# Performance work log

Hardware: AMD Instinct MI355X
Metric: run time of the kernel (lower is better)

The kernel has to match this reference:

```python
import jax, jax.numpy as jnp
import numpy as np

N_NODES = 100000
N_EDGES = 3200000
IN_F = 128
OUT_F = 64
HEADS = 8
ALPHA = 0.2  # LeakyReLU negative slope


def setup_inputs() -> dict:
    key = jax.random.key(0)
    k1, k2, k3, k4 = jax.random.split(key, 4)
    x = jax.random.normal(k1, (N_NODES, IN_F), dtype=jnp.float32)
    edges = jax.random.randint(k2, (2, N_EDGES), 0, N_NODES, dtype=jnp.int64)
    # glorot-uniform-ish scaled params, stacked over heads
    lim_W = np.sqrt(6.0 / (IN_F + OUT_F))
    lim_a = np.sqrt(6.0 / (2 * OUT_F + 1))
    W = jax.random.uniform(k3, (HEADS, IN_F, OUT_F), minval=-lim_W, maxval=lim_W, dtype=jnp.float32)
    a = jax.random.uniform(k4, (HEADS, 2 * OUT_F, 1), minval=-lim_a, maxval=lim_a, dtype=jnp.float32)
    return {"x": x, "edges": edges, "W": W, "a": a}


def reference(x, edges, W, a):
    # x: [N, in_f]; edges: [2, E]; W: [H, in_f, out_f]; a: [H, 2*out_f, 1]
    N = x.shape[0]
    src, tgt = edges[0], edges[1]
    outs = []
    for h in range(W.shape[0]):  # small fixed head count; keeps peak memory per-head
        Wh = x @ W[h]                                  # [N, F]
        # Whij @ a == Wh[src] @ a[:F] + Wh[tgt] @ a[F:], computed at node level
        a_src = Wh @ a[h, :OUT_F, 0]                   # [N]
        a_tgt = Wh @ a[h, OUT_F:, 0]                   # [N]
        e = -jax.nn.leaky_relu(a_src[src] + a_tgt[tgt], negative_slope=ALPHA)  # [E]
        e_exp = jnp.exp(e - jnp.max(e))                # global max, as in the torch code
        denom = jax.ops.segment_sum(e_exp, src, num_segments=N) + 1e-10  # [N]
        att = e_exp / denom[src]                       # [E] edge softmax over source groups
        msg = att[:, None] * Wh[tgt]                   # [E, F]
        outs.append(jax.ops.segment_sum(msg, src, num_segments=N))  # [N, F]
    return jnp.concatenate(outs, axis=1)               # concat reduction -> [N, H*F]
```

## Files before the change

### kernel.cpp

```cpp
#include <hip/hip_runtime.h>
#include <hip/hip_bf16.h>

#define N_NODES 100000
#define N_EDGES 3200000
#define IN_F 128
#define OUT_F 64
#define HEADS 8
#define ALPHA 0.2f

#define BSHIFT 7
#define NBUCK 782
#define CHUNK 2048
#define NPBLK 1563
#define XADOT_BLKS 1024

typedef __bf16 bf16x8 __attribute__((ext_vector_type(8)));
typedef float f32x4 __attribute__((ext_vector_type(4)));
typedef __attribute__((ext_vector_type(8))) unsigned short ushort8;

static __device__ __forceinline__ unsigned short f2b(float f) {
    __hip_bfloat16 h = __float2bfloat16(f);
    return __builtin_bit_cast(unsigned short, h);
}

static __device__ __forceinline__ void gll16(const void* g, void* l) {
    __builtin_amdgcn_global_load_lds(
        (const __attribute__((address_space(1))) void*)g,
        (__attribute__((address_space(3))) void*)l, 16, 0, 0);
}

__global__ __launch_bounds__(256) void k_prep(const float* __restrict__ W,
                                              const float* __restrict__ a,
                                              unsigned short* __restrict__ Wt,
                                              float* __restrict__ uvT,
                                              int* __restrict__ bhist) {
    int b = blockIdx.x, t = threadIdx.x;
    if (b < 256) {
        int idx = b * 256 + t;
        int k = idx & 127;
        int c = idx >> 7;
        int h = c >> 6;
        int f = c & 63;
        Wt[idx] = f2b(W[h * IN_F * OUT_F + k * OUT_F + f]);
    } else if (b == 256) {
#pragma unroll
        for (int j = 0; j < 4; ++j) {
            int t2 = t + j * 256;
            int h = t2 >> 7, k = t2 & 127;
            const float* Wrow = W + h * IN_F * OUT_F + k * OUT_F;
            const float* ah = a + h * 2 * OUT_F;
            float su = 0.f, sv = 0.f;
            for (int f = 0; f < OUT_F; ++f) {
                float wv = Wrow[f];
                su += wv * ah[f];
                sv += wv * ah[OUT_F + f];
            }
            uvT[k * 16 + h] = su;
            uvT[k * 16 + 8 + h] = sv;
        }
    } else {
        for (int i = t; i < NBUCK; i += 256) bhist[i] = 0;
    }
}

__global__ __launch_bounds__(256) void k_xadot(const float* __restrict__ x,
                                               const float* __restrict__ uvT,
                                               const int* __restrict__ src,
                                               unsigned short* __restrict__ xb,
                                               float* __restrict__ asrc,
                                               float* __restrict__ atgt,
                                               int* __restrict__ bhist) {
    const int b = blockIdx.x, t = threadIdx.x;
    if (b >= XADOT_BLKS) {
        __shared__ int h[NBUCK];
        for (int i = t; i < NBUCK; i += 256) h[i] = 0;
        __syncthreads();
        int cb = b - XADOT_BLKS;
        int i0 = cb * CHUNK;
        int iend = i0 + CHUNK;
        if (iend > N_EDGES) iend = N_EDGES;
        for (int i = i0 + t; i < iend; i += 256)
            atomicAdd(&h[src[i] >> BSHIFT], 1);
        __syncthreads();
        for (int i = t; i < NBUCK; i += 256)
            if (h[i]) atomicAdd(&bhist[i], h[i]);
        return;
    }
    const int lane = t & 63, wid = t >> 6;
    const int o = lane & 15, q = lane >> 4;
    float up[32];
#pragma unroll
    for (int j = 0; j < 32; ++j) up[j] = uvT[(q * 32 + j) * 16 + o];

    for (int n = b * 4 + wid; n < N_NODES; n += XADOT_BLKS * 4) {
        const float* xr = x + (size_t)n * 128;
        float2 xv2 = *reinterpret_cast<const float2*>(xr + 2 * lane);
        ushort2 pv = make_ushort2(f2b(xv2.x), f2b(xv2.y));
        *reinterpret_cast<ushort2*>(xb + (size_t)n * 128 + 2 * lane) = pv;
        float r = 0.f;
        const float4* xq = reinterpret_cast<const float4*>(xr + q * 32);
#pragma unroll
        for (int j = 0; j < 8; ++j) {
            float4 xv = xq[j];
            r = fmaf(xv.x, up[4 * j], r);
            r = fmaf(xv.y, up[4 * j + 1], r);
            r = fmaf(xv.z, up[4 * j + 2], r);
            r = fmaf(xv.w, up[4 * j + 3], r);
        }
        r += __shfl_xor(r, 16);
        r += __shfl_xor(r, 32);
        if (lane < 8) asrc[n * 8 + o] = r;
        else if (lane < 16) atgt[n * 8 + (o - 8)] = r;
    }
}

__global__ __launch_bounds__(1024) void k_bscan(const int* __restrict__ bhist,
                                                int* __restrict__ bstart,
                                                int* __restrict__ bcursor,
                                                int* __restrict__ rowptr) {
    __shared__ int s[1024];
    int t = threadIdx.x;
    int v = (t < NBUCK) ? bhist[t] : 0;
    s[t] = v;
    __syncthreads();
    for (int d = 1; d < 1024; d <<= 1) {
        int add = (t >= d) ? s[t - d] : 0;
        __syncthreads();
        s[t] += add;
        __syncthreads();
    }
    if (t < NBUCK) {
        int st = s[t] - v;
        bstart[t] = st;
        bcursor[t] = st;
    }
    if (t == 0) {
        bstart[NBUCK] = N_EDGES;
        rowptr[N_NODES] = N_EDGES;
    }
}

__global__ __launch_bounds__(256) void k_bscatter(const int* __restrict__ src,
                                                  const int* __restrict__ tgt,
                                                  int* __restrict__ bcursor,
                                                  unsigned int* __restrict__ pairs) {
    __shared__ int h[NBUCK];
    __shared__ int rsv[NBUCK];
    for (int i = threadIdx.x; i < NBUCK; i += 256) h[i] = 0;
    __syncthreads();
    int i0 = blockIdx.x * CHUNK;
    int iend = i0 + CHUNK;
    if (iend > N_EDGES) iend = N_EDGES;
    for (int i = i0 + threadIdx.x; i < iend; i += 256)
        atomicAdd(&h[src[i] >> BSHIFT], 1);
    __syncthreads();
    for (int i = threadIdx.x; i < NBUCK; i += 256) {
        int c = h[i];
        rsv[i] = c ? atomicAdd(&bcursor[i], c) : 0;
        h[i] = 0;
    }
    __syncthreads();
    for (int i = i0 + threadIdx.x; i < iend; i += 256) {
        int s = src[i];
        int b = s >> BSHIFT;
        int p = rsv[b] + atomicAdd(&h[b], 1);
        pairs[p] = ((unsigned)(s & 127) << 17) | (unsigned)tgt[i];
    }
}

__global__ __launch_bounds__(512) void k_bsort(const unsigned int* __restrict__ pairs,
                                               const int* __restrict__ bstart,
                                               int* __restrict__ rowptr,
                                               int* __restrict__ stgt) {
    __shared__ int h[128];
    __shared__ int s[128];
    int b = blockIdx.x;
    int p0 = bstart[b], p1 = bstart[b + 1];
    int n0 = b << BSHIFT;
    int t = threadIdx.x;
    if (t < 128) h[t] = 0;
    __syncthreads();
    for (int i = p0 + t; i < p1; i += 512)
        atomicAdd(&h[pairs[i] >> 17], 1);
    __syncthreads();
    int v = (t < 128) ? h[t] : 0;
    if (t < 128) s[t] = v;
    __syncthreads();
    for (int d = 1; d < 128; d <<= 1) {
        int add = (t >= d && t < 128) ? s[t - d] : 0;
        __syncthreads();
        if (t < 128) s[t] += add;
        __syncthreads();
    }
    if (t < 128) {
        int pos = p0 + s[t] - v;
        int node = n0 + t;
        if (node < N_NODES) rowptr[node] = pos;
        h[t] = pos;
    }
    __syncthreads();
    for (int i = p0 + t; i < p1; i += 512) {
        unsigned int pr = pairs[i];
        int pos = atomicAdd(&h[pr >> 17], 1);
        stgt[pos] = (int)(pr & 0x1FFFF);
    }
}

__global__ __launch_bounds__(256) void k_agg10(const int* __restrict__ rowptr,
                                               const int* __restrict__ stgt,
                                               const float* __restrict__ asrc,
                                               const float* __restrict__ atgt,
                                               const unsigned short* __restrict__ xb,
                                               unsigned short* __restrict__ aggout) {
    __shared__ char lds[4 * 5120];
    const int tid = threadIdx.x;
    const int wid = tid >> 6, lane = tid & 63;
    const int node = blockIdx.x * 4 + wid;
    if (node >= N_NODES) return;
    const int seg = lane & 15;
    const int hp = lane >> 4;
    const int base = rowptr[node], end = rowptr[node + 1];
    const float2 asr = *reinterpret_cast<const float2*>(asrc + (size_t)node * 8 + hp * 2);
    char* buf = lds + wid * 5120;

    float2 accA[4] = {}, accB[4] = {};
    float den0 = 0.f, den1 = 0.f;

    const int deg = end - base;
    const int nch = (deg + 15) >> 4;

    auto eidx = [&](int c) {
        int i = base + c * 16 + seg;
        if (i >= end) i = end - 1;
        return i;
    };
    auto stage = [&](int t16) {
        int te_a = __shfl(t16, (lane & 31) >> 1);
        gll16(atgt + (size_t)te_a * 8 + (lane & 1) * 4, buf);
#pragma unroll
        for (int p = 0; p < 4; ++p) {
            int te = __shfl(t16, p * 4 + hp);
            gll16(xb + (size_t)te * 128 + seg * 8, buf + 1024 + p * 1024);
        }
    };

#define EDGE_STEP(E) { \
        uint4 xu = *reinterpret_cast<const uint4*>(Xb + (E) * 256 + seg * 16); \
        float2 w2 = *reinterpret_cast<const float2*>(buf + (E) * 32 + hp * 8); \
        _Pragma("unroll") \
        for (int i = 0; i < 4; ++i) { \
            unsigned int u = (&xu.x)[i]; \
            float2 xv; \
            xv.x = __builtin_bit_cast(float, u << 16); \
            xv.y = __builtin_bit_cast(float, u & 0xFFFF0000u); \
            asm("v_pk_fma_f32 %0, %1, %2, %0 op_sel:[0,0,0] op_sel_hi:[1,0,1]" \
                : "+v"(accA[i]) : "v"(xv), "v"(w2)); \
            asm("v_pk_fma_f32 %0, %1, %2, %0 op_sel:[0,1,0] op_sel_hi:[1,1,1]" \
                : "+v"(accB[i]) : "v"(xv), "v"(w2)); \
        } }

    if (nch > 0) {
        int t16 = stgt[eidx(0)];
        for (int c = 0; c < nch; ++c) {
            asm volatile("s_waitcnt lgkmcnt(0)" ::: "memory");
            __builtin_amdgcn_sched_barrier(0);
            stage(t16);
            if (c + 1 < nch) t16 = stgt[eidx(c + 1)];
            asm volatile("s_waitcnt vmcnt(0)" ::: "memory");
            __builtin_amdgcn_sched_barrier(0);
            int c0 = base + c * 16;
            int cnt = end - c0;
            if (cnt > 16) cnt = 16;
            {
                float2 at2 = *reinterpret_cast<const float2*>(buf + seg * 32 + hp * 8);
                float z0 = asr.x + at2.x, z1 = asr.y + at2.y;
                float e0 = (z0 > 0.f) ? -z0 : -(ALPHA * z0);
                float e1 = (z1 > 0.f) ? -z1 : -(ALPHA * z1);
                bool ok = seg < cnt;
                float w0 = ok ? __expf(e0) : 0.f;
                float w1 = ok ? __expf(e1) : 0.f;
                den0 += w0;
                den1 += w1;
                float2 wout = {w0, w1};
                *reinterpret_cast<float2*>(buf + seg * 32 + hp * 8) = wout;
            }
            asm volatile("s_waitcnt lgkmcnt(0)" ::: "memory");
            __builtin_amdgcn_sched_barrier(0);
            const char* Xb = buf + 1024;
            if (cnt == 16) {
#pragma unroll 4
                for (int e = 0; e < 16; ++e) EDGE_STEP(e)
            } else {
                for (int e = 0; e < cnt; ++e) EDGE_STEP(e)
            }
        }
    }
#undef EDGE_STEP

    for (int d = 1; d <= 8; d <<= 1) {
        den0 += __shfl_xor(den0, d);
        den1 += __shfl_xor(den1, d);
    }
    float invA = 1.f / (den0 + 1e-10f);
    float invB = 1.f / (den1 + 1e-10f);
    ushort8 oA, oB;
#pragma unroll
    for (int i = 0; i < 4; ++i) {
        oA[2 * i] = f2b(accA[i].x * invA);
        oA[2 * i + 1] = f2b(accA[i].y * invA);
        oB[2 * i] = f2b(accB[i].x * invB);
        oB[2 * i + 1] = f2b(accB[i].y * invB);
    }
    unsigned short* op = aggout + (size_t)node * 1024 + (hp * 2) * 128 + seg * 8;
    *reinterpret_cast<ushort8*>(op) = oA;
    *reinterpret_cast<ushort8*>(op + 128) = oB;
}

#define LDK2 136
__global__ __launch_bounds__(256) void k_gemm2(const unsigned short* __restrict__ agg,
                                               const unsigned short* __restrict__ Wt,
                                               float* __restrict__ out) {
    __shared__ unsigned short Al[128 * LDK2];
    __shared__ unsigned short Bl[64 * LDK2];
    const int tid = threadIdx.x;
    const int h = blockIdx.y;
    const int r0 = blockIdx.x * 128;
    for (int it = 0; it < 8; ++it) {
        int idx = tid + it * 256;
        int r = idx >> 4, k8 = (idx & 15) << 3;
        int gr = r0 + r;
        if (gr >= N_NODES) gr = N_NODES - 1;
        *reinterpret_cast<ushort8*>(&Al[r * LDK2 + k8]) =
            *reinterpret_cast<const ushort8*>(agg + (size_t)gr * 1024 + h * 128 + k8);
    }
    for (int it = 0; it < 4; ++it) {
        int idx = tid + it * 256;
        int f = idx >> 4, k8 = (idx & 15) << 3;
        *reinterpret_cast<ushort8*>(&Bl[f * LDK2 + k8]) =
            *reinterpret_cast<const ushort8*>(Wt + (size_t)(h * 64 + f) * 128 + k8);
    }
    __syncthreads();
    const int lane = tid & 63, w = tid >> 6;
    const int l15 = lane & 15, lq = lane >> 4;
    f32x4 acc[2][4] = {};
    for (int ks = 0; ks < 4; ++ks) {
        int koff = ks * 32 + lq * 8;
        bf16x8 af0 = *reinterpret_cast<const bf16x8*>(&Al[(w * 32 + l15) * LDK2 + koff]);
        bf16x8 af1 = *reinterpret_cast<const bf16x8*>(&Al[(w * 32 + 16 + l15) * LDK2 + koff]);
#pragma unroll
        for (int n = 0; n < 4; ++n) {
            bf16x8 bf_ = *reinterpret_cast<const bf16x8*>(&Bl[(n * 16 + l15) * LDK2 + koff]);
            acc[0][n] = __builtin_amdgcn_mfma_f32_16x16x32_bf16(af0, bf_, acc[0][n], 0, 0, 0);
            acc[1][n] = __builtin_amdgcn_mfma_f32_16x16x32_bf16(af1, bf_, acc[1][n], 0, 0, 0);
        }
    }
#pragma unroll
    for (int m = 0; m < 2; ++m)
#pragma unroll
        for (int n = 0; n < 4; ++n) {
            int col = h * 64 + n * 16 + l15;
            int rbase = r0 + w * 32 + m * 16 + lq * 4;
#pragma unroll
            for (int r2 = 0; r2 < 4; ++r2) {
                int rr = rbase + r2;
                if (rr < N_NODES) out[(size_t)rr * 512 + col] = acc[m][n][r2];
            }
        }
}

extern "C" void kernel_launch(void* const* d_in, const int* in_sizes, int n_in,
                              void* d_out, int out_size, void* d_ws, size_t ws_size,
                              hipStream_t stream) {
    const float* x = (const float*)d_in[0];
    const int* edges = (const int*)d_in[1];
    const float* W = (const float*)d_in[2];
    const float* a = (const float*)d_in[3];
    float* out = (float*)d_out;
    const int* src = edges;
    const int* tgt = edges + N_EDGES;

    char* ws = (char*)d_ws;
    size_t off = 0;
    auto alloc = [&](size_t bytes) -> void* {
        void* p = (void*)(ws + off);
        off += (bytes + 255) & ~(size_t)255;
        return p;
    };
    unsigned short* Wt = (unsigned short*)alloc((size_t)HEADS * OUT_F * IN_F * 2);
    float* uvT = (float*)alloc((size_t)IN_F * 16 * 4);
    unsigned short* xb = (unsigned short*)alloc((size_t)N_NODES * IN_F * 2);
    float* asrc = (float*)alloc((size_t)N_NODES * 8 * 4);
    float* atgt = (float*)alloc((size_t)N_NODES * 8 * 4);
    int* bhist = (int*)alloc((size_t)NBUCK * 4);
    int* bstart = (int*)alloc((size_t)(NBUCK + 1) * 4);
    int* bcursor = (int*)alloc((size_t)NBUCK * 4);
    int* rowptr = (int*)alloc((size_t)(N_NODES + 1) * 4);
    unsigned int* pairs = (unsigned int*)alloc((size_t)N_EDGES * 4);
    int* stgt = (int*)alloc((size_t)N_EDGES * 4);
    (void)ws_size; (void)n_in; (void)in_sizes; (void)out_size;

    k_prep<<<258, 256, 0, stream>>>(W, a, Wt, uvT, bhist);
    k_xadot<<<XADOT_BLKS + NPBLK, 256, 0, stream>>>(x, uvT, src, xb, asrc, atgt, bhist);
    k_bscan<<<1, 1024, 0, stream>>>(bhist, bstart, bcursor, rowptr);
    k_bscatter<<<NPBLK, 256, 0, stream>>>(src, tgt, bcursor, pairs);
    k_bsort<<<NBUCK, 512, 0, stream>>>(pairs, bstart, rowptr, stgt);
    k_agg10<<<25000, 256, 0, stream>>>(rowptr, stgt, asrc, atgt, xb,
                                       (unsigned short*)d_out);
    k_gemm2<<<dim3(782, 8), 256, 0, stream>>>((const unsigned short*)d_out, Wt, out);
}
```

Measured before the change: 455.8 us.

## Fuse CSR build stages into one cooperative kernel with grid syncs

Replaces the separate histogram, scan, scatter and bucket-sort launches with a single cooperative kernel that runs each stage with grid-wide syncs. The histogram is no longer co-scheduled inside the x-projection kernel. The aim is to cut launch gaps and kernel-boundary overhead between the small sort stages. In exchange, the histogram loses its overlap with k_xadot, only 512 blocks run each stage, and each grid.sync has its own cost.

```diff
diff --git a/kernel.cpp b/kernel.cpp
--- a/kernel.cpp
+++ b/kernel.cpp
@@ -1,5 +1,8 @@
 #include <hip/hip_runtime.h>
 #include <hip/hip_bf16.h>
+#include <hip/hip_cooperative_groups.h>
+
+namespace cg = cooperative_groups;
 
 #define N_NODES 100000
 #define N_EDGES 3200000
@@ -11,8 +14,8 @@
 #define BSHIFT 7
 #define NBUCK 782
 #define CHUNK 2048
-#define NPBLK 1563
-#define XADOT_BLKS 1024
+#define NCHUNK 1563
+#define CHAIN_BLKS 512
 
 typedef __bf16 bf16x8 __attribute__((ext_vector_type(8)));
 typedef float f32x4 __attribute__((ext_vector_type(4)));
@@ -32,8 +35,7 @@
 __global__ __launch_bounds__(256) void k_prep(const float* __restrict__ W,
                                               const float* __restrict__ a,
                                               unsigned short* __restrict__ Wt,
-                                              float* __restrict__ uvT,
-                                              int* __restrict__ bhist) {
+                                              float* __restrict__ uvT) {
     int b = blockIdx.x, t = threadIdx.x;
     if (b < 256) {
         int idx = b * 256 + t;
@@ -42,7 +44,7 @@
         int h = c >> 6;
         int f = c & 63;
         Wt[idx] = f2b(W[h * IN_F * OUT_F + k * OUT_F + f]);
-    } else if (b == 256) {
+    } else {
 #pragma unroll
         for (int j = 0; j < 4; ++j) {
             int t2 = t + j * 256;
@@ -58,41 +60,22 @@
             uvT[k * 16 + h] = su;
             uvT[k * 16 + 8 + h] = sv;
         }
-    } else {
-        for (int i = t; i < NBUCK; i += 256) bhist[i] = 0;
     }
 }
 
 __global__ __launch_bounds__(256) void k_xadot(const float* __restrict__ x,
                                                const float* __restrict__ uvT,
-                                               const int* __restrict__ src,
                                                unsigned short* __restrict__ xb,
                                                float* __restrict__ asrc,
-                                               float* __restrict__ atgt,
-                                               int* __restrict__ bhist) {
+                                               float* __restrict__ atgt) {
     const int b = blockIdx.x, t = threadIdx.x;
-    if (b >= XADOT_BLKS) {
-        __shared__ int h[NBUCK];
-        for (int i = t; i < NBUCK; i += 256) h[i] = 0;
-        __syncthreads();
-        int cb = b - XADOT_BLKS;
-        int i0 = cb * CHUNK;
-        int iend = i0 + CHUNK;
-        if (iend > N_EDGES) iend = N_EDGES;
-        for (int i = i0 + t; i < iend; i += 256)
-            atomicAdd(&h[src[i] >> BSHIFT], 1);
-        __syncthreads();
-        for (int i = t; i < NBUCK; i += 256)
-            if (h[i]) atomicAdd(&bhist[i], h[i]);
-        return;
-    }
     const int lane = t & 63, wid = t >> 6;
     const int o = lane & 15, q = lane >> 4;
     float up[32];
 #pragma unroll
     for (int j = 0; j < 32; ++j) up[j] = uvT[(q * 32 + j) * 16 + o];
 
-    for (int n = b * 4 + wid; n < N_NODES; n += XADOT_BLKS * 4) {
+    for (int n = b * 4 + wid; n < N_NODES; n += 1024 * 4) {
         const float* xr = x + (size_t)n * 128;
         float2 xv2 = *reinterpret_cast<const float2*>(xr + 2 * lane);
         ushort2 pv = make_ushort2(f2b(xv2.x), f2b(xv2.y));
@@ -114,95 +97,125 @@
     }
 }
 
-__global__ __launch_bounds__(1024) void k_bscan(const int* __restrict__ bhist,
-                                                int* __restrict__ bstart,
-                                                int* __restrict__ bcursor,
-                                                int* __restrict__ rowptr) {
-    __shared__ int s[1024];
-    int t = threadIdx.x;
-    int v = (t < NBUCK) ? bhist[t] : 0;
-    s[t] = v;
-    __syncthreads();
-    for (int d = 1; d < 1024; d <<= 1) {
-        int add = (t >= d) ? s[t - d] : 0;
-        __syncthreads();
-        s[t] += add;
-        __syncthreads();
-    }
-    if (t < NBUCK) {
-        int st = s[t] - v;
-        bstart[t] = st;
-        bcursor[t] = st;
-    }
-    if (t == 0) {
-        bstart[NBUCK] = N_EDGES;
-        rowptr[N_NODES] = N_EDGES;
-    }
-}
-
-__global__ __launch_bounds__(256) void k_bscatter(const int* __restrict__ src,
-                                                  const int* __restrict__ tgt,
-                                                  int* __restrict__ bcursor,
-                                                  unsigned int* __restrict__ pairs) {
-    __shared__ int h[NBUCK];
-    __shared__ int rsv[NBUCK];
-    for (int i = threadIdx.x; i < NBUCK; i += 256) h[i] = 0;
-    __syncthreads();
-    int i0 = blockIdx.x * CHUNK;
-    int iend = i0 + CHUNK;
-    if (iend > N_EDGES) iend = N_EDGES;
-    for (int i = i0 + threadIdx.x; i < iend; i += 256)
-        atomicAdd(&h[src[i] >> BSHIFT], 1);
-    __syncthreads();
-    for (int i = threadIdx.x; i < NBUCK; i += 256) {
-        int c = h[i];
-        rsv[i] = c ? atomicAdd(&bcursor[i], c) : 0;
-        h[i] = 0;
-    }
-    __syncthreads();
-    for (int i = i0 + threadIdx.x; i < iend; i += 256) {
-        int s = src[i];
-        int b = s >> BSHIFT;
-        int p = rsv[b] + atomicAdd(&h[b], 1);
-        pairs[p] = ((unsigned)(s & 127) << 17) | (unsigned)tgt[i];
-    }
-}
-
-__global__ __launch_bounds__(512) void k_bsort(const unsigned int* __restrict__ pairs,
-                                               const int* __restrict__ bstart,
+__global__ __launch_bounds__(512) void k_chain(const int* __restrict__ src,
+                                               const int* __restrict__ tgt,
+                                               int* __restrict__ bhist,
+                                               int* __restrict__ bstart,
+                                               int* __restrict__ bcursor,
                                                int* __restrict__ rowptr,
+                                               unsigned int* __restrict__ pairs,
                                                int* __restrict__ stgt) {
-    __shared__ int h[128];
-    __shared__ int s[128];
-    int b = blockIdx.x;
-    int p0 = bstart[b], p1 = bstart[b + 1];
-    int n0 = b << BSHIFT;
-    int t = threadIdx.x;
-    if (t < 128) h[t] = 0;
-    __syncthreads();
-    for (int i = p0 + t; i < p1; i += 512)
-        atomicAdd(&h[pairs[i] >> 17], 1);
-    __syncthreads();
-    int v = (t < 128) ? h[t] : 0;
-    if (t < 128) s[t] = v;
-    __syncthreads();
-    for (int d = 1; d < 128; d <<= 1) {
-        int add = (t >= d && t < 128) ? s[t - d] : 0;
-        __syncthreads();
-        if (t < 128) s[t] += add;
-        __syncthreads();
-    }
-    if (t < 128) {
-        int pos = p0 + s[t] - v;
-        int node = n0 + t;
-        if (node < N_NODES) rowptr[node] = pos;
-        h[t] = pos;
-    }
-    __syncthreads();
-    for (int i = p0 + t; i < p1; i += 512) {
-        unsigned int pr = pairs[i];
-        int pos = atomicAdd(&h[pr >> 17], 1);
-        stgt[pos] = (int)(pr & 0x1FFFF);
+    cg::grid_group grid = cg::this_grid();
+    __shared__ int shm[2 * NBUCK];
+    const int b = blockIdx.x, t = threadIdx.x;
+
+    for (int i = b * 512 + t; i < NBUCK; i += CHAIN_BLKS * 512) bhist[i] = 0;
+    grid.sync();
+
+    for (int cb = b; cb < NCHUNK; cb += CHAIN_BLKS) {
+        for (int i = t; i < NBUCK; i += 512) shm[i] = 0;
+        __syncthreads();
+        int i0 = cb * CHUNK;
+        int iend = i0 + CHUNK;
+        if (iend > N_EDGES) iend = N_EDGES;
+        for (int i = i0 + t; i < iend; i += 512)
+            atomicAdd(&shm[src[i] >> BSHIFT], 1);
+        __syncthreads();
+        for (int i = t; i < NBUCK; i += 512)
+            if (shm[i]) atomicAdd(&bhist[i], shm[i]);
+        __syncthreads();
+    }
+    grid.sync();
+
+    if (b == 0) {
+        int v0 = (t < NBUCK) ? bhist[t] : 0;
+        int v1 = (t + 512 < NBUCK) ? bhist[t + 512] : 0;
+        shm[t] = v0;
+        shm[t + 512] = v1;
+        __syncthreads();
+        for (int d = 1; d < 1024; d <<= 1) {
+            int a0 = (t >= d) ? shm[t - d] : 0;
+            int a1 = (t + 512 >= d) ? shm[t + 512 - d] : 0;
+            __syncthreads();
+            shm[t] += a0;
+            shm[t + 512] += a1;
+            __syncthreads();
+        }
+        if (t < NBUCK) {
+            int st = shm[t] - v0;
+            bstart[t] = st;
+            bcursor[t] = st;
+        }
+        if (t + 512 < NBUCK) {
+            int st = shm[t + 512] - v1;
+            bstart[t + 512] = st;
+            bcursor[t + 512] = st;
+        }
+        if (t == 0) {
+            bstart[NBUCK] = N_EDGES;
+            rowptr[N_NODES] = N_EDGES;
+        }
+    }
+    grid.sync();
+
+    int* h = shm;
+    int* rsv = shm + NBUCK;
+    for (int cb = b; cb < NCHUNK; cb += CHAIN_BLKS) {
+        for (int i = t; i < NBUCK; i += 512) h[i] = 0;
+        __syncthreads();
+        int i0 = cb * CHUNK;
+        int iend = i0 + CHUNK;
+        if (iend > N_EDGES) iend = N_EDGES;
+        for (int i = i0 + t; i < iend; i += 512)
+            atomicAdd(&h[src[i] >> BSHIFT], 1);
+        __syncthreads();
+        for (int i = t; i < NBUCK; i += 512) {
+            int c = h[i];
+            rsv[i] = c ? atomicAdd(&bcursor[i], c) : 0;
+            h[i] = 0;
+        }
+        __syncthreads();
+        for (int i = i0 + t; i < iend; i += 512) {
+            int s = src[i];
+            int bk = s >> BSHIFT;
+            int p = rsv[bk] + atomicAdd(&h[bk], 1);
+            pairs[p] = ((unsigned)(s & 127) << 17) | (unsigned)tgt[i];
+        }
+        __syncthreads();
+    }
+    grid.sync();
+
+    int* s2 = shm + 128;
+    for (int bk = b; bk < NBUCK; bk += CHAIN_BLKS) {
+        int p0 = bstart[bk], p1 = bstart[bk + 1];
+        int n0 = bk << BSHIFT;
+        if (t < 128) h[t] = 0;
+        __syncthreads();
+        for (int i = p0 + t; i < p1; i += 512)
+            atomicAdd(&h[pairs[i] >> 17], 1);
+        __syncthreads();
+        int v = (t < 128) ? h[t] : 0;
+        if (t < 128) s2[t] = v;
+        __syncthreads();
+        for (int d = 1; d < 128; d <<= 1) {
+            int add = (t >= d && t < 128) ? s2[t - d] : 0;
+            __syncthreads();
+            if (t < 128) s2[t] += add;
+            __syncthreads();
+        }
+        if (t < 128) {
+            int pos = p0 + s2[t] - v;
+            int node = n0 + t;
+            if (node < N_NODES) rowptr[node] = pos;
+            h[t] = pos;
+        }
+        __syncthreads();
+        for (int i = p0 + t; i < p1; i += 512) {
+            unsigned int pr = pairs[i];
+            int pos = atomicAdd(&h[pr >> 17], 1);
+            stgt[pos] = (int)(pr & 0x1FFFF);
+        }
+        __syncthreads();
     }
 }
 
@@ -399,11 +412,14 @@
     int* stgt = (int*)alloc((size_t)N_EDGES * 4);
     (void)ws_size; (void)n_in; (void)in_sizes; (void)out_size;
 
-    k_prep<<<258, 256, 0, stream>>>(W, a, Wt, uvT, bhist);
-    k_xadot<<<XADOT_BLKS + NPBLK, 256, 0, stream>>>(x, uvT, src, xb, asrc, atgt, bhist);
-    k_bscan<<<1, 1024, 0, stream>>>(bhist, bstart, bcursor, rowptr);
-    k_bscatter<<<NPBLK, 256, 0, stream>>>(src, tgt, bcursor, pairs);
-    k_bsort<<<NBUCK, 512, 0, stream>>>(pairs, bstart, rowptr, stgt);
+    k_prep<<<257, 256, 0, stream>>>(W, a, Wt, uvT);
+    k_xadot<<<1024, 256, 0, stream>>>(x, uvT, xb, asrc, atgt);
+    {
+        void* cargs[] = {(void*)&src, (void*)&tgt, (void*)&bhist, (void*)&bstart,
+                         (void*)&bcursor, (void*)&rowptr, (void*)&pairs, (void*)&stgt};
+        hipLaunchCooperativeKernel((const void*)k_chain, dim3(CHAIN_BLKS), dim3(512),
+                                   cargs, 0, stream);
+    }
     k_agg10<<<25000, 256, 0, stream>>>(rowptr, stgt, asrc, atgt, xb,
                                        (unsigned short*)d_out);
     k_gemm2<<<dim3(782, 8), 256, 0, stream>>>((const unsigned short*)d_out, Wt, out);
```

After: 618.3 us. 35.7% more time.
